# Performance work log

Measured on AMD Instinct MI355X. Metric: run time of the kernel, lower is better.

The kernel has to match this reference:

```python
import jax, jax.numpy as jnp
import numpy as np

LABEL_SMOOTHING = 0.1


def setup_inputs() -> dict:
    key = jax.random.key(0)
    k1, k2, k3 = jax.random.split(key, 3)
    B, N, D = 16384, 1000, 1000  # code structurally requires D == n_classes == N
    inputs = jax.random.uniform(k1, (B, D), dtype=jnp.float32)
    labels = jax.random.randint(k2, (B,), 0, N, dtype=jnp.int64)
    code_book = jax.random.uniform(k3, (N, D), dtype=jnp.float32)
    return {"inputs": inputs, "labels": labels, "code_book": code_book}


def reference(inputs, labels, code_book):
    # inputs: [B, D], code_book: [N, D], D == N (n_classes)
    n_classes = inputs.shape[1]
    # soft targets with label smoothing (same as scatter_ + smoothing)
    soft_target = jax.nn.one_hot(labels, n_classes, dtype=inputs.dtype)
    soft_target = soft_target * (1.0 - LABEL_SMOOTHING) + LABEL_SMOOTHING / n_classes
    # Hamming similarity: sum_d [o*c + (1-o)*(1-c)]  ==  o@c.T + (1-o)@(1-c).T
    # (algebraic rewrite of the [B, N, D] broadcast in the original; same math)
    similarity = (jnp.einsum("bd,nd->bn", inputs, code_book)
                  + jnp.einsum("bd,nd->bn", 1.0 - inputs, 1.0 - code_book))
    logp = jax.nn.log_softmax(similarity, axis=1)
    return jnp.mean(jnp.sum(-soft_target * logp, axis=1))
```

## Files before the change

### kernel.cpp

```cpp
#include <hip/hip_runtime.h>

typedef __attribute__((ext_vector_type(8))) short bf16x8;
typedef __attribute__((ext_vector_type(4))) float f32x4;

#define AS1 __attribute__((address_space(1)))
#define AS3 __attribute__((address_space(3)))

__device__ static inline void gl2lds16(const void* g, void* l) {
  __builtin_amdgcn_global_load_lds((const AS1 unsigned int*)g, (AS3 unsigned int*)l, 16, 0, 0);
}

__device__ static inline unsigned short f2bf(float x) {
  unsigned int u = __float_as_uint(x);
  unsigned int r = u + 0x7FFFu + ((u >> 16) & 1u);
  return (unsigned short)(r >> 16);
}

__global__ __launch_bounds__(256) void prep_inputs_k(const float* __restrict__ in,
                                                     unsigned short* __restrict__ a) {
  int idx = blockIdx.x * 256 + threadIdx.x;
  int row = idx >> 7;
  int g   = idx & 127;
  union { unsigned short u[8]; uint4 v; } pk;
  if (g < 125) {
    const float4* p = (const float4*)(in + (size_t)row * 1000 + g * 8);
    float4 v0 = p[0], v1 = p[1];
    pk.u[0] = f2bf(2.f * v0.x); pk.u[1] = f2bf(2.f * v0.y);
    pk.u[2] = f2bf(2.f * v0.z); pk.u[3] = f2bf(2.f * v0.w);
    pk.u[4] = f2bf(2.f * v1.x); pk.u[5] = f2bf(2.f * v1.y);
    pk.u[6] = f2bf(2.f * v1.z); pk.u[7] = f2bf(2.f * v1.w);
  } else {
    pk.v = make_uint4(0, 0, 0, 0);
  }
  *(uint4*)(a + ((size_t)row << 10) + (g << 3)) = pk.v;
}

__global__ __launch_bounds__(256) void prep_code_k(const float* __restrict__ cb,
                                                   unsigned short* __restrict__ b,
                                                   float* __restrict__ rowsum) {
  int n = blockIdx.x;
  int t = threadIdx.x;
  float s = 0.f;
#pragma unroll
  for (int j = 0; j < 4; ++j) {
    int c = t + j * 256;
    float v = 0.f;
    if (n < 1000 && c < 1000) v = cb[(size_t)n * 1000 + c];
    s += v;
    b[((size_t)n << 10) + c] = f2bf(v);
  }
  __shared__ float red[256];
  red[t] = s;
  __syncthreads();
  for (int o = 128; o > 0; o >>= 1) {
    if (t < o) red[t] += red[t + o];
    __syncthreads();
  }
  if (t == 0) rowsum[n] = (n < 1000) ? red[0] : 0.f;
}

__global__ __launch_bounds__(256) void fix_labels_k(const int* __restrict__ raw,
                                                    int* __restrict__ labs) {
  __shared__ int nz;
  int t = threadIdx.x;
  if (t == 0) nz = 0;
  __syncthreads();
  if (raw[2 * t + 1] != 0) atomicAdd(&nz, 1);
  __syncthreads();
  bool is64 = (nz < 32);
  int row = blockIdx.x * 256 + t;
  labs[row] = is64 ? raw[2 * row] : raw[row];
}

__global__ __launch_bounds__(256, 2) void coding_loss_k(
    const unsigned short* __restrict__ A,
    const unsigned short* __restrict__ B,
    const float* __restrict__ rowsum,
    const int* __restrict__ labels,
    float* __restrict__ Z,
    float* __restrict__ lin) {
  __shared__ __align__(16) unsigned char lds[49152 + 1040];
  unsigned short* buf = (unsigned short*)lds;
  float* zbuf = (float*)(lds + 49152);
  float* lbuf = zbuf + 256;

  const int t    = threadIdx.x;
  const int lane = t & 63;
  const int w    = t >> 6;
  const int wr   = w >> 1;
  const int wc   = w & 1;
  const int g16  = lane >> 4;
  const int c16  = lane & 15;
  const int ct   = blockIdx.x & 3;
  const int rt   = blockIdx.x >> 2;
  const int r0   = rt << 7;
  const int c0   = ct << 8;

  size_t a_src[2]; int a_dst[2];
#pragma unroll
  for (int i = 0; i < 2; ++i) {
    int ch = i * 256 + t, row = ch >> 2;
    int sg = (ch & 3) ^ ((row >> 1) & 3);
    a_src[i] = (size_t)(r0 + row) * 1024 + sg * 8;
    a_dst[i] = 8192 + ch * 8;
  }
  size_t b_src[4]; int b_dst[4];
#pragma unroll
  for (int i = 0; i < 4; ++i) {
    int ch = i * 256 + t, row = ch >> 2;
    int sg = (ch & 3) ^ ((row >> 1) & 3);
    b_src[i] = (size_t)(c0 + row) * 1024 + sg * 8;
    b_dst[i] = ch * 8;
  }

  int a_eoff[4], b_eoff[8];
#pragma unroll
  for (int mi = 0; mi < 4; ++mi) {
    int ar = wr * 64 + mi * 16 + c16;
    a_eoff[mi] = 8192 + ar * 32 + ((g16 ^ ((ar >> 1) & 3)) << 3);
  }
#pragma unroll
  for (int ni = 0; ni < 8; ++ni) {
    int br = wc * 128 + ni * 16 + c16;
    b_eoff[ni] = br * 32 + ((g16 ^ ((br >> 1) & 3)) << 3);
  }

  f32x4 acc[4][8];
#pragma unroll
  for (int mi = 0; mi < 4; ++mi)
#pragma unroll
    for (int ni = 0; ni < 8; ++ni) acc[mi][ni] = (f32x4)(0.f);

#pragma unroll
  for (int i = 0; i < 2; ++i) gl2lds16(A + a_src[i], buf + a_dst[i]);
#pragma unroll
  for (int i = 0; i < 4; ++i) gl2lds16(B + b_src[i], buf + b_dst[i]);
  __syncthreads();

  int p = 0;
  for (int k0 = 0; k0 < 1024; k0 += 32) {
    if (k0 + 32 < 1024) {
      unsigned short* np = buf + (p ^ 1) * 12288;
#pragma unroll
      for (int i = 0; i < 2; ++i) gl2lds16(A + a_src[i] + k0 + 32, np + a_dst[i]);
#pragma unroll
      for (int i = 0; i < 4; ++i) gl2lds16(B + b_src[i] + k0 + 32, np + b_dst[i]);
    }
    const unsigned short* bp = buf + p * 12288;
    bf16x8 af[4], bf[8];
#pragma unroll
    for (int mi = 0; mi < 4; ++mi) af[mi] = *(const bf16x8*)(bp + a_eoff[mi]);
#pragma unroll
    for (int ni = 0; ni < 8; ++ni) bf[ni] = *(const bf16x8*)(bp + b_eoff[ni]);
#pragma unroll
    for (int mi = 0; mi < 4; ++mi)
#pragma unroll
      for (int ni = 0; ni < 8; ++ni)
        acc[mi][ni] = __builtin_amdgcn_mfma_f32_16x16x32_bf16(af[mi], bf[ni], acc[mi][ni], 0, 0, 0);
    __syncthreads();
    p ^= 1;
  }

  float rs[8]; int colg[8];
#pragma unroll
  for (int ni = 0; ni < 8; ++ni) {
    colg[ni] = c0 + wc * 128 + ni * 16 + c16;
    rs[ni]   = rowsum[colg[ni]];
  }
  float lacc = 0.f;
  float ez[4][4];
#pragma unroll
  for (int mi = 0; mi < 4; ++mi)
#pragma unroll
    for (int r = 0; r < 4; ++r) {
      int labv = labels[r0 + wr * 64 + mi * 16 + g16 * 4 + r];
      float e = 0.f;
#pragma unroll
      for (int ni = 0; ni < 8; ++ni) {
        float S = acc[mi][ni][r] - rs[ni];
        e += __expf(S - 40.f);
        lacc += 1e-4f * S;
        if (colg[ni] == labv) lacc += 0.9f * S;
      }
      ez[mi][r] = e;
    }
#pragma unroll
  for (int d = 1; d < 16; d <<= 1)
#pragma unroll
    for (int mi = 0; mi < 4; ++mi)
#pragma unroll
      for (int r = 0; r < 4; ++r) ez[mi][r] += __shfl_xor(ez[mi][r], d, 64);
  if (c16 == 0) {
#pragma unroll
    for (int mi = 0; mi < 4; ++mi)
#pragma unroll
      for (int r = 0; r < 4; ++r) zbuf[w * 64 + mi * 16 + g16 * 4 + r] = ez[mi][r];
  }
#pragma unroll
  for (int d = 1; d < 64; d <<= 1) lacc += __shfl_xor(lacc, d, 64);
  if (lane == 0) lbuf[w] = lacc;
  __syncthreads();
  if (t < 128) {
    int wrg = t >> 6, lr = t & 63;
    float z = zbuf[(wrg * 2 + 0) * 64 + lr] + zbuf[(wrg * 2 + 1) * 64 + lr];
    Z[ct * 16384 + r0 + t] = z;
  }
  if (t == 0) atomicAdd(lin, lbuf[0] + lbuf[1] + lbuf[2] + lbuf[3]);
}

__global__ __launch_bounds__(256) void finalize_k(const float* __restrict__ Z,
                                                  const float* __restrict__ lin,
                                                  float* __restrict__ out) {
  int t = threadIdx.x;
  int row = blockIdx.x * 256 + t;
  float v = 40.f + logf(Z[row] + Z[16384 + row] + Z[2 * 16384 + row] + Z[3 * 16384 + row]);
#pragma unroll
  for (int d = 1; d < 64; d <<= 1) v += __shfl_xor(v, d, 64);
  __shared__ float s[4];
  if ((t & 63) == 0) s[t >> 6] = v;
  __syncthreads();
  if (t == 0) {
    float tot = s[0] + s[1] + s[2] + s[3];
    if (blockIdx.x == 0) tot -= lin[0];
    atomicAdd(out, tot * (1.f / 16384.f));
  }
}

extern "C" void kernel_launch(void* const* d_in, const int* in_sizes, int n_in,
                              void* d_out, int out_size, void* d_ws, size_t ws_size,
                              hipStream_t stream) {
  const float* inputs = (const float*)d_in[0];
  const int* labraw   = (const int*)d_in[1];
  const float* code   = (const float*)d_in[2];

  unsigned short* a_bf = (unsigned short*)d_ws;
  unsigned short* b_bf = a_bf + (size_t)16384 * 1024;
  float* rowsum        = (float*)(b_bf + (size_t)1024 * 1024);
  float* Z             = rowsum + 1024;
  float* lin           = Z + 4 * 16384;
  int* labs            = (int*)(lin + 1);

  hipMemsetAsync(lin, 0, sizeof(float), stream);
  hipMemsetAsync(d_out, 0, sizeof(float), stream);
  fix_labels_k<<<64, 256, 0, stream>>>(labraw, labs);
  prep_inputs_k<<<8192, 256, 0, stream>>>(inputs, a_bf);
  prep_code_k<<<1024, 256, 0, stream>>>(code, b_bf, rowsum);
  coding_loss_k<<<512, 256, 0, stream>>>(a_bf, b_bf, rowsum, labs, Z, lin);
  finalize_k<<<64, 256, 0, stream>>>(Z, lin, (float*)d_out);
}
```

Before: 149.8 us.

## Triple-buffer A and double-buffer B tiles with explicit vmcnt waits

Reworks the GEMM main loop's LDS staging so that A tiles use three buffers (prefetched two steps ahead) and B tiles use two buffers. Explicit s_waitcnt on vmcnt replaces the full __syncthreads so that outstanding async global-to-LDS loads can stay in flight while MFMAs run. The goal is to hide more global load latency. In exchange, LDS use grows from about 49KB to 57KB per block, which may pressure the 2-blocks-per-CU occupancy. The correctness of the hand-counted waitcnt values is delicate.

```diff
diff --git a/kernel.cpp b/kernel.cpp
--- a/kernel.cpp
+++ b/kernel.cpp
@@ -79,9 +79,13 @@
     const int* __restrict__ labels,
     float* __restrict__ Z,
     float* __restrict__ lin) {
-  __shared__ __align__(16) unsigned char lds[49152 + 1040];
-  unsigned short* buf = (unsigned short*)lds;
-  float* zbuf = (float*)(lds + 49152);
+  __shared__ __align__(16) unsigned char lds[24576 + 32768 + 1040];
+  unsigned short* Ab0 = (unsigned short*)lds;
+  unsigned short* Ab1 = Ab0 + 4096;
+  unsigned short* Ab2 = Ab1 + 4096;
+  unsigned short* Bb0 = Ab2 + 4096;
+  unsigned short* Bb1 = Bb0 + 8192;
+  float* zbuf = (float*)(lds + 57344);
   float* lbuf = zbuf + 256;
 
   const int t    = threadIdx.x;
@@ -102,7 +106,7 @@
     int ch = i * 256 + t, row = ch >> 2;
     int sg = (ch & 3) ^ ((row >> 1) & 3);
     a_src[i] = (size_t)(r0 + row) * 1024 + sg * 8;
-    a_dst[i] = 8192 + ch * 8;
+    a_dst[i] = ch * 8;
   }
   size_t b_src[4]; int b_dst[4];
 #pragma unroll
@@ -117,7 +121,7 @@
 #pragma unroll
   for (int mi = 0; mi < 4; ++mi) {
     int ar = wr * 64 + mi * 16 + c16;
-    a_eoff[mi] = 8192 + ar * 32 + ((g16 ^ ((ar >> 1) & 3)) << 3);
+    a_eoff[mi] = ar * 32 + ((g16 ^ ((ar >> 1) & 3)) << 3);
   }
 #pragma unroll
   for (int ni = 0; ni < 8; ++ni) {
@@ -131,34 +135,52 @@
 #pragma unroll
     for (int ni = 0; ni < 8; ++ni) acc[mi][ni] = (f32x4)(0.f);
 
-#pragma unroll
-  for (int i = 0; i < 2; ++i) gl2lds16(A + a_src[i], buf + a_dst[i]);
-#pragma unroll
-  for (int i = 0; i < 4; ++i) gl2lds16(B + b_src[i], buf + b_dst[i]);
-  __syncthreads();
-
-  int p = 0;
-  for (int k0 = 0; k0 < 1024; k0 += 32) {
-    if (k0 + 32 < 1024) {
-      unsigned short* np = buf + (p ^ 1) * 12288;
-#pragma unroll
-      for (int i = 0; i < 2; ++i) gl2lds16(A + a_src[i] + k0 + 32, np + a_dst[i]);
-#pragma unroll
-      for (int i = 0; i < 4; ++i) gl2lds16(B + b_src[i] + k0 + 32, np + b_dst[i]);
-    }
-    const unsigned short* bp = buf + p * 12288;
-    bf16x8 af[4], bf[8];
-#pragma unroll
-    for (int mi = 0; mi < 4; ++mi) af[mi] = *(const bf16x8*)(bp + a_eoff[mi]);
-#pragma unroll
-    for (int ni = 0; ni < 8; ++ni) bf[ni] = *(const bf16x8*)(bp + b_eoff[ni]);
-#pragma unroll
-    for (int mi = 0; mi < 4; ++mi)
-#pragma unroll
-      for (int ni = 0; ni < 8; ++ni)
-        acc[mi][ni] = __builtin_amdgcn_mfma_f32_16x16x32_bf16(af[mi], bf[ni], acc[mi][ni], 0, 0, 0);
-    __syncthreads();
-    p ^= 1;
+#define STAGE_A(kk, dst) \
+  { _Pragma("unroll") for (int i = 0; i < 2; ++i) gl2lds16(A + a_src[i] + (kk) * 32, (dst) + a_dst[i]); }
+#define STAGE_B(kk, dst) \
+  { _Pragma("unroll") for (int i = 0; i < 4; ++i) gl2lds16(B + b_src[i] + (kk) * 32, (dst) + b_dst[i]); }
+#define COMPUTE(pa, pb)                                                                   \
+  {                                                                                       \
+    bf16x8 af[4], bf[8];                                                                  \
+    _Pragma("unroll") for (int mi = 0; mi < 4; ++mi) af[mi] = *(const bf16x8*)((pa) + a_eoff[mi]); \
+    _Pragma("unroll") for (int ni = 0; ni < 8; ++ni) bf[ni] = *(const bf16x8*)((pb) + b_eoff[ni]); \
+    _Pragma("unroll") for (int mi = 0; mi < 4; ++mi)                                      \
+      _Pragma("unroll") for (int ni = 0; ni < 8; ++ni)                                    \
+        acc[mi][ni] = __builtin_amdgcn_mfma_f32_16x16x32_bf16(af[mi], bf[ni], acc[mi][ni], 0, 0, 0); \
+  }
+#define WAITVM(n) __builtin_amdgcn_s_waitcnt(0xF70 | (n))
+
+  STAGE_A(0, Ab0);
+  STAGE_B(0, Bb0);
+  STAGE_A(1, Ab1);
+
+  unsigned short *pa_cur = Ab0, *pa_nxt = Ab1, *pa_stg = Ab2;
+  unsigned short *pb_cur = Bb0, *pb_stg = Bb1;
+
+#pragma unroll 2
+  for (int kc = 0; kc < 30; ++kc) {
+    STAGE_B(kc + 1, pb_stg);
+    STAGE_A(kc + 2, pa_stg);
+    WAITVM(8);
+    __builtin_amdgcn_s_barrier();
+    COMPUTE(pa_cur, pb_cur);
+    __builtin_amdgcn_s_barrier();
+    unsigned short* tmp = pa_cur; pa_cur = pa_nxt; pa_nxt = pa_stg; pa_stg = tmp;
+    tmp = pb_cur; pb_cur = pb_stg; pb_stg = tmp;
+  }
+  {
+    STAGE_B(31, pb_stg);
+    WAITVM(6);
+    __builtin_amdgcn_s_barrier();
+    COMPUTE(pa_cur, pb_cur);
+    __builtin_amdgcn_s_barrier();
+    unsigned short* tmp = pa_cur; pa_cur = pa_nxt; pa_nxt = tmp;
+    tmp = pb_cur; pb_cur = pb_stg; pb_stg = tmp;
+  }
+  {
+    WAITVM(0);
+    __builtin_amdgcn_s_barrier();
+    COMPUTE(pa_cur, pb_cur);
   }
 
   float rs[8]; int colg[8];
@@ -206,6 +228,10 @@
     Z[ct * 16384 + r0 + t] = z;
   }
   if (t == 0) atomicAdd(lin, lbuf[0] + lbuf[1] + lbuf[2] + lbuf[3]);
+#undef STAGE_A
+#undef STAGE_B
+#undef COMPUTE
+#undef WAITVM
 }
 
 __global__ __launch_bounds__(256) void finalize_k(const float* __restrict__ Z,
```

New measurement: 148.5 us. No clear change (-0.9%).
